# Kernel optimization log

Measured on AMD Instinct MI355X. Metric: run time of the kernel, lower is better.

Reference implementation:

```python
import jax, jax.numpy as jnp
import numpy as np

H, W, C, B = 16, 16, 2048, 32
HEADS = 4
D1, D2 = 256, 128


def _build_edges(h, w):
    """Lattice + mirror + disease-node + self-loop edges (PyG GATConv default adds self loops)."""
    idx = lambda i, j: i * w + j
    edges = []
    for i in range(h):
        for j in range(w):
            if i + 1 < h:
                edges += [(idx(i, j), idx(i + 1, j)), (idx(i + 1, j), idx(i, j))]
            if j + 1 < w:
                edges += [(idx(i, j), idx(i, j + 1)), (idx(i, j + 1), idx(i, j))]
            mj = w - j - 1
            if mj != j:
                edges.append((idx(i, j), idx(i, mj)))
    n = h * w
    for i in range(n):  # disease node (index n), bidirectional
        edges += [(i, n), (n, i)]
    for i in range(n + 1):  # self loops
        edges.append((i, i))
    e = np.asarray(edges, dtype=np.int32)
    return jnp.asarray(e[:, 0]), jnp.asarray(e[:, 1])


def setup_inputs() -> dict:
    key = jax.random.key(0)
    ks = jax.random.split(key, 16)
    s = 0.02
    src, dst = _build_edges(H, W)
    return {
        "fmap": jax.random.normal(ks[0], (B, C, H, W), jnp.float32),
        "W1": jax.random.normal(ks[1], (C, HEADS * D1), jnp.float32) * s,
        "a_src1": jax.random.normal(ks[2], (HEADS, D1), jnp.float32) * s,
        "a_dst1": jax.random.normal(ks[3], (HEADS, D1), jnp.float32) * s,
        "b1": jnp.zeros((D1,), jnp.float32),
        "W2": jax.random.normal(ks[4], (D1, HEADS * D2), jnp.float32) * s,
        "a_src2": jax.random.normal(ks[5], (HEADS, D2), jnp.float32) * s,
        "a_dst2": jax.random.normal(ks[6], (HEADS, D2), jnp.float32) * s,
        "b2": jnp.zeros((D2,), jnp.float32),
        "Wp": jax.random.normal(ks[7], (D2, 1), jnp.float32) * s,
        "bp": jnp.zeros((1,), jnp.float32),
        "Wc1": jax.random.normal(ks[8], (D2, 64), jnp.float32) * s,
        "bc1": jnp.zeros((64,), jnp.float32),
        "Wc2": jax.random.normal(ks[9], (64, 1), jnp.float32) * s,
        "bc2": jnp.zeros((1,), jnp.float32),
        "src": src,
        "dst": dst,
    }


def _gat_layer(x, src, dst, Wm, a_s, a_d, b, heads, out_dim):
    """PyG GATConv math: concat=False (mean over heads), leaky_relu slope 0.2."""
    N = x.shape[0]
    h = (x @ Wm).reshape(N, heads, out_dim)           # [N, H, D]
    es = jnp.sum(h * a_s, axis=-1)                    # [N, H]
    ed = jnp.sum(h * a_d, axis=-1)                    # [N, H]
    e = jax.nn.leaky_relu(es[src] + ed[dst], 0.2)     # [E, H]
    m = jax.ops.segment_max(e, dst, num_segments=N)   # softmax over incoming edges
    alpha = jnp.exp(e - m[dst])
    denom = jax.ops.segment_sum(alpha, dst, num_segments=N)
    alpha = alpha / (denom[dst] + 1e-16)
    agg = jax.ops.segment_sum(alpha[:, :, None] * h[src], dst, num_segments=N)
    return agg.mean(axis=1) + b                       # [N, D]


def reference(fmap, W1, a_src1, a_dst1, b1, W2, a_src2, a_dst2, b2,
              Wp, bp, Wc1, bc1, Wc2, bc2, src, dst):
    Bn, Cc, Hh, Ww = fmap.shape
    nodes = fmap.reshape(Bn, Cc, Hh * Ww).transpose(0, 2, 1)   # [B, HW, C]
    nodes = jnp.concatenate([nodes, jnp.zeros((Bn, 1, Cc), nodes.dtype)], axis=1)

    def per_graph(x):
        x = _gat_layer(x, src, dst, W1, a_src1, a_dst1, b1, HEADS, D1)
        x = _gat_layer(x, src, dst, W2, a_src2, a_dst2, b2, HEADS, D2)
        w = jax.nn.sigmoid(x @ Wp + bp)               # [N, 1] attention pool weights
        g = jnp.mean(x * w, axis=0)                   # global_mean_pool, single graph
        h1 = jax.nn.relu(g @ Wc1 + bc1)
        pred = jax.nn.sigmoid(h1 @ Wc2 + bc2)         # [1]
        return pred[0], w[:, 0]

    preds, atts = jax.vmap(per_graph)(nodes)          # [B], [B, N]
    return preds, atts
```

## Files before the change

### kernel.cpp

```cpp
#include <hip/hip_runtime.h>

typedef __bf16 bf16_t;
typedef __bf16 bf16x8 __attribute__((ext_vector_type(8)));
typedef float f32x4 __attribute__((ext_vector_type(4)));

#define MPAD  8320
#define NNODE 257
#define NB    32

__device__ __forceinline__ void gld_lds16(const bf16_t* g, bf16_t* l) {
    __builtin_amdgcn_global_load_lds(
        (const __attribute__((address_space(1))) void*)g,
        (__attribute__((address_space(3))) void*)l, 16, 0, 0);
}

__global__ __launch_bounds__(256) void setup_kernel(const float* __restrict__ W1, bf16_t* __restrict__ W1t,
                                                    const float* __restrict__ W2, bf16_t* __restrict__ W2t,
                                                    const float* __restrict__ fmap, bf16_t* __restrict__ X,
                                                    const int* __restrict__ dstv, int E,
                                                    int* __restrict__ indptr, int* __restrict__ eidx,
                                                    float* __restrict__ zbase, bf16_t* __restrict__ out1) {
    __shared__ float smem[64 * 65];
    int idx = blockIdx.x, t = threadIdx.x;
    if (idx < 2176) {
        const float* W; bf16_t* Wt; int K, N, kt, nt;
        if (idx < 2048) { W = W1; Wt = W1t; K = 2048; N = 1024; kt = idx >> 5; nt = idx & 31; }
        else { int l = idx - 2048; W = W2; Wt = W2t; K = 256; N = 512; kt = l >> 4; nt = l & 15; }
        int k0 = kt * 32, n0 = nt * 32;
        int tx = t & 31, ty = t >> 5;
#pragma unroll
        for (int i = 0; i < 4; i++)
            smem[(ty + i * 8) * 33 + tx] = W[(size_t)(k0 + ty + i * 8) * N + n0 + tx];
        __syncthreads();
#pragma unroll
        for (int i = 0; i < 4; i++)
            Wt[(size_t)(n0 + ty + i * 8) * K + k0 + tx] = (bf16_t)smem[tx * 33 + ty + i * 8];
    } else if (idx < 6272) {
        int local = idx - 2176;
        int ct = local & 31, rem = local >> 5;
        int nt = rem & 3, b = rem >> 2;
        int c0 = ct * 64, n0 = nt * 64;
        const float* f = fmap + (size_t)b * 2048 * 256;
        int ln = t & 63, lc = t >> 6;
#pragma unroll
        for (int i = 0; i < 16; i++) {
            int c = lc + i * 4;
            smem[c * 65 + ln] = f[(size_t)(c0 + c) * 256 + n0 + ln];
        }
        __syncthreads();
        int sn = t >> 3, sc = (t & 7) * 8;
#pragma unroll
        for (int half = 0; half < 2; half++) {
            int n = sn + half * 32;
            bf16_t tmp[8];
#pragma unroll
            for (int j = 0; j < 8; j++) tmp[j] = (bf16_t)smem[(sc + j) * 65 + n];
            *(bf16x8*)&X[(size_t)(b * 257 + n0 + n) * 2048 + c0 + sc] = *(bf16x8*)tmp;
        }
    } else if (idx < 6402) {
        int local = idx - 6272;
        uint4* p = (uint4*)zbase + (size_t)local * 256;
        p[t] = uint4{0, 0, 0, 0};
    } else if (idx < 6530) {
        int i = idx - 6402;
        int row = (i < 32) ? (i * 257 + 256) : (8224 + (i - 32));
        uint4* p = (uint4*)(X + (size_t)row * 2048);
        p[t] = uint4{0, 0, 0, 0};
    } else if (idx < 6542) {
        int local = idx - 6530;
        uint4* p = (uint4*)((char*)(out1 + (size_t)8224 * 256) + (size_t)local * 4096);
        p[t] = uint4{0, 0, 0, 0};
    } else {
        __shared__ int cnt[258];
        __shared__ int off[258];
        for (int i = t; i < 258; i += 256) cnt[i] = 0;
        __syncthreads();
        for (int e = t; e < E; e += 256) atomicAdd(&cnt[dstv[e] + 1], 1);
        __syncthreads();
        if (t == 0) {
            int s = 0;
            for (int i = 0; i < 258; i++) { s += cnt[i]; off[i] = s; }
        }
        __syncthreads();
        for (int i = t; i < 258; i += 256) indptr[i] = off[i];
        __syncthreads();
        for (int e = t; e < E; e += 256) {
            int p = atomicAdd(&off[dstv[e]], 1);
            eidx[p] = e;
        }
    }
}

__global__ __launch_bounds__(128, 2) void gemm_kernel(const bf16_t* __restrict__ A,
                                                      const bf16_t* __restrict__ Bt,
                                                      bf16_t* __restrict__ C,
                                                      const float* __restrict__ asrc,
                                                      const float* __restrict__ adst,
                                                      float* __restrict__ es,
                                                      float* __restrict__ ed,
                                                      int K, int N, int headD) {
    __shared__ __align__(16) bf16_t sm[3 * 8192];
    int row0 = blockIdx.y * 128, col0 = blockIdx.x * 128;
    int t = threadIdx.x;
    int wave = t >> 6, lane = t & 63;
    int srow = lane >> 2, scol = (lane & 3) * 8;
    const bf16_t* Abase = A + (size_t)row0 * K;
    const bf16_t* Bbase = Bt + (size_t)col0 * K;
    f32x4 acc[4][8] = {};
    int fr = lane & 15;
    int kq = (lane >> 4) * 8;
    int nk = K >> 5;
    auto issue = [&](int kt, int stage) {
        bf16_t* As = sm + stage * 8192;
        bf16_t* Bs = As + 4096;
        int k0 = kt << 5;
#pragma unroll
        for (int c = 0; c < 4; c++) {
            int chunk = wave * 4 + c;
            int row = chunk * 16 + srow;
            gld_lds16(Abase + (size_t)row * K + k0 + scol, &As[chunk * 512]);
            gld_lds16(Bbase + (size_t)row * K + k0 + scol, &Bs[chunk * 512]);
        }
    };
    issue(0, 0);
    if (nk > 1) issue(1, 1);
    for (int k = 0; k < nk; k++) {
        int cur = k % 3;
        if (k + 2 < nk) {
            issue(k + 2, (k + 2) % 3);
            asm volatile("s_waitcnt vmcnt(16)" ::: "memory");
        } else if (k + 1 < nk) {
            asm volatile("s_waitcnt vmcnt(8)" ::: "memory");
        } else {
            asm volatile("s_waitcnt vmcnt(0)" ::: "memory");
        }
        __builtin_amdgcn_s_barrier();
        const bf16_t* As = sm + cur * 8192;
        const bf16_t* Bs = As + 4096;
        bf16x8 af[4], bfv[8];
#pragma unroll
        for (int mr = 0; mr < 4; mr++)
            af[mr] = *(const bf16x8*)&As[(wave * 64 + mr * 16 + fr) * 32 + kq];
#pragma unroll
        for (int nc = 0; nc < 8; nc++)
            bfv[nc] = *(const bf16x8*)&Bs[(nc * 16 + fr) * 32 + kq];
#pragma unroll
        for (int mr = 0; mr < 4; mr++)
#pragma unroll
            for (int nc = 0; nc < 8; nc++)
                acc[mr][nc] = __builtin_amdgcn_mfma_f32_16x16x32_bf16(
                    af[mr], bfv[nc], acc[mr][nc], 0, 0, 0);
        asm volatile("s_waitcnt lgkmcnt(0)" ::: "memory");
        __builtin_amdgcn_s_barrier();
    }
#pragma unroll
    for (int mr = 0; mr < 4; mr++) {
        int crow = row0 + wave * 64 + mr * 16 + (lane >> 4) * 4;
#pragma unroll
        for (int nc = 0; nc < 8; nc++) {
            int ccol = col0 + nc * 16 + (lane & 15);
#pragma unroll
            for (int r = 0; r < 4; r++)
                C[(size_t)(crow + r) * N + ccol] = (bf16_t)acc[mr][nc][r];
        }
    }
    int h = col0 / headD;
    float as_v[8], ad_v[8];
#pragma unroll
    for (int nc = 0; nc < 8; nc++) {
        int ccol = col0 + nc * 16 + (lane & 15);
        as_v[nc] = asrc[ccol];
        ad_v[nc] = adst[ccol];
    }
#pragma unroll
    for (int mr = 0; mr < 4; mr++)
#pragma unroll
        for (int r = 0; r < 4; r++) {
            float ps = 0.f, pd = 0.f;
#pragma unroll
            for (int nc = 0; nc < 8; nc++) {
                float v = acc[mr][nc][r];
                ps += v * as_v[nc];
                pd += v * ad_v[nc];
            }
#pragma unroll
            for (int m = 1; m < 16; m <<= 1) {
                ps += __shfl_xor(ps, m);
                pd += __shfl_xor(pd, m);
            }
            if ((lane & 15) == 0) {
                int row = row0 + wave * 64 + mr * 16 + (lane >> 4) * 4 + r;
                atomicAdd(&es[row * 4 + h], ps);
                atomicAdd(&ed[row * 4 + h], pd);
            }
        }
}

template<int D>
__global__ __launch_bounds__(256) void attn_kernel(const bf16_t* __restrict__ Hb,
                                                   const float* __restrict__ es,
                                                   const float* __restrict__ ed,
                                                   const int* __restrict__ indptr,
                                                   const int* __restrict__ eidx,
                                                   const int* __restrict__ srcv,
                                                   const float* __restrict__ bias,
                                                   float* __restrict__ outf,
                                                   bf16_t* __restrict__ outb) {
    constexpr int VPL = D / 64;
    int d = blockIdx.x, b = blockIdx.y;
    int r = b * 257 + d;
    int t = threadIdx.x, wv = t >> 6, lane = t & 63;
    int e0 = indptr[d];
    int deg = indptr[d + 1] - e0;
    __shared__ float alpha[NNODE * 4];
    __shared__ int   ssh[NNODE];
    __shared__ float wred[4][8];
    __shared__ float mh4[4], rh4[4];
    __shared__ float osh[4][D];
    const float4 edv = *(const float4*)&ed[r * 4];
    float edh[4] = {edv.x, edv.y, edv.z, edv.w};
    float lmax[4] = {-1e30f, -1e30f, -1e30f, -1e30f};
    for (int i = t; i < deg; i += 256) {
        int s = srcv[eidx[e0 + i]];
        ssh[i] = s;
        float4 e4 = *(const float4*)&es[(b * 257 + s) * 4];
        float ev[4] = {e4.x, e4.y, e4.z, e4.w};
#pragma unroll
        for (int h = 0; h < 4; h++) {
            float v = ev[h] + edh[h];
            v = v > 0.f ? v : 0.2f * v;
            alpha[i * 4 + h] = v;
            lmax[h] = fmaxf(lmax[h], v);
        }
    }
#pragma unroll
    for (int h = 0; h < 4; h++) {
        float m = lmax[h];
#pragma unroll
        for (int o = 32; o > 0; o >>= 1) m = fmaxf(m, __shfl_down(m, o));
        if (lane == 0) wred[h][wv] = m;
    }
    __syncthreads();
    if (t < 4)
        mh4[t] = fmaxf(fmaxf(wred[t][0], wred[t][1]), fmaxf(wred[t][2], wred[t][3]));
    __syncthreads();
    float lsum[4] = {0.f, 0.f, 0.f, 0.f};
    for (int i = t; i < deg; i += 256) {
#pragma unroll
        for (int h = 0; h < 4; h++) {
            float a = __expf(alpha[i * 4 + h] - mh4[h]);
            alpha[i * 4 + h] = a;
            lsum[h] += a;
        }
    }
#pragma unroll
    for (int h = 0; h < 4; h++) {
        float s = lsum[h];
#pragma unroll
        for (int o = 32; o > 0; o >>= 1) s += __shfl_down(s, o);
        if (lane == 0) wred[h][wv] = s;
    }
    __syncthreads();
    if (t < 4)
        rh4[t] = 1.f / (wred[t][0] + wred[t][1] + wred[t][2] + wred[t][3] + 1e-16f);
    __syncthreads();
    float rh = rh4[wv];
    float acc[VPL] = {};
    const bf16_t* hb = Hb + (size_t)(b * 257) * 4 * D + wv * D + lane * VPL;
    for (int i = 0; i < deg; i++) {
        float a = alpha[i * 4 + wv] * rh;
        const bf16_t* hr = hb + (size_t)ssh[i] * 4 * D;
        bf16_t xv[VPL];
        __builtin_memcpy(xv, hr, VPL * 2);
#pragma unroll
        for (int v = 0; v < VPL; v++) acc[v] += a * (float)xv[v];
    }
#pragma unroll
    for (int v = 0; v < VPL; v++) osh[wv][lane * VPL + v] = acc[v];
    __syncthreads();
    if (t < D) {
        float o = (osh[0][t] + osh[1][t] + osh[2][t] + osh[3][t]) * 0.25f + bias[t];
        if (outb) outb[(size_t)r * D + t] = (bf16_t)o;
        else      outf[(size_t)r * D + t] = o;
    }
}

__global__ __launch_bounds__(256) void head_kernel(const float* __restrict__ out2,
                                                   const float* __restrict__ Wp,
                                                   const float* __restrict__ bp,
                                                   const float* __restrict__ Wc1,
                                                   const float* __restrict__ bc1,
                                                   const float* __restrict__ Wc2,
                                                   const float* __restrict__ bc2,
                                                   float* __restrict__ outp) {
    int b = blockIdx.x, t = threadIdx.x, wv = t >> 6, lane = t & 63;
    __shared__ float wsh[NNODE];
    __shared__ float gpart[2][128];
    __shared__ float gsh[128];
    __shared__ float h1[64];
    const float* X = out2 + (size_t)b * 257 * 128;
    float wp0 = Wp[lane], wp1 = Wp[64 + lane], bp0 = bp[0];
    for (int n = wv; n < 257; n += 4) {
        const float* xr = X + n * 128;
        float s = xr[lane] * wp0 + xr[64 + lane] * wp1;
#pragma unroll
        for (int o = 32; o > 0; o >>= 1) s += __shfl_down(s, o);
        if (lane == 0) {
            float wvv = 1.f / (1.f + __expf(-(s + bp0)));
            wsh[n] = wvv;
            outp[32 + b * 257 + n] = wvv;
        }
    }
    __syncthreads();
    {
        int dim = t & 127, half = t >> 7;
        float s = 0.f;
        for (int n = half; n < 257; n += 2) s += X[n * 128 + dim] * wsh[n];
        gpart[half][dim] = s;
    }
    __syncthreads();
    if (t < 128) gsh[t] = (gpart[0][t] + gpart[1][t]) * (1.f / 257.f);
    __syncthreads();
    if (t < 64) {
        float s = bc1[t];
        for (int k = 0; k < 128; k++) s += gsh[k] * Wc1[k * 64 + t];
        h1[t] = fmaxf(s, 0.f);
    }
    __syncthreads();
    if (t == 0) {
        float s = bc2[0];
        for (int j = 0; j < 64; j++) s += h1[j] * Wc2[j];
        outp[b] = 1.f / (1.f + expf(-s));
    }
}

extern "C" void kernel_launch(void* const* d_in, const int* in_sizes, int n_in,
                              void* d_out, int out_size, void* d_ws, size_t ws_size,
                              hipStream_t stream) {
    const float* fmap   = (const float*)d_in[0];
    const float* W1     = (const float*)d_in[1];
    const float* a_src1 = (const float*)d_in[2];
    const float* a_dst1 = (const float*)d_in[3];
    const float* b1     = (const float*)d_in[4];
    const float* W2     = (const float*)d_in[5];
    const float* a_src2 = (const float*)d_in[6];
    const float* a_dst2 = (const float*)d_in[7];
    const float* b2     = (const float*)d_in[8];
    const float* Wp     = (const float*)d_in[9];
    const float* bp     = (const float*)d_in[10];
    const float* Wc1    = (const float*)d_in[11];
    const float* bc1    = (const float*)d_in[12];
    const float* Wc2    = (const float*)d_in[13];
    const float* bc2    = (const float*)d_in[14];
    const int*   srcv   = (const int*)d_in[15];
    const int*   dstv   = (const int*)d_in[16];
    int E = in_sizes[15];
    float* outp = (float*)d_out;

    char* w = (char*)d_ws;
    size_t off = 0;
    auto alloc = [&](size_t bytes) -> void* {
        void* p = w + off;
        off += (bytes + 255) & ~(size_t)255;
        return p;
    };
    bf16_t* X    = (bf16_t*)alloc((size_t)MPAD * 2048 * sizeof(bf16_t));
    bf16_t* W1t  = (bf16_t*)alloc((size_t)1024 * 2048 * sizeof(bf16_t));
    bf16_t* W2t  = (bf16_t*)alloc((size_t)512 * 256 * sizeof(bf16_t));
    bf16_t* H1   = (bf16_t*)alloc((size_t)MPAD * 1024 * sizeof(bf16_t));
    bf16_t* out1 = (bf16_t*)alloc((size_t)MPAD * 256 * sizeof(bf16_t));
    bf16_t* H2   = (bf16_t*)alloc((size_t)MPAD * 512 * sizeof(bf16_t));
    float*  out2 = (float*)alloc((size_t)MPAD * 128 * sizeof(float));
    float*  es1  = (float*)alloc((size_t)MPAD * 4 * sizeof(float));
    float*  ed1  = (float*)alloc((size_t)MPAD * 4 * sizeof(float));
    float*  es2  = (float*)alloc((size_t)MPAD * 4 * sizeof(float));
    float*  ed2  = (float*)alloc((size_t)MPAD * 4 * sizeof(float));
    int*  indptr = (int*)alloc(258 * sizeof(int));
    int*  eidx   = (int*)alloc((size_t)E * sizeof(int));

    setup_kernel<<<6543, 256, 0, stream>>>(W1, W1t, W2, W2t, fmap, X, dstv, E,
                                           indptr, eidx, es1, out1);
    gemm_kernel<<<dim3(1024 / 128, MPAD / 128), 128, 0, stream>>>(
        X, W1t, H1, a_src1, a_dst1, es1, ed1, 2048, 1024, 256);
    attn_kernel<256><<<dim3(NNODE, NB), 256, 0, stream>>>(H1, es1, ed1, indptr, eidx,
                                                          srcv, b1, nullptr, out1);
    gemm_kernel<<<dim3(512 / 128, MPAD / 128), 128, 0, stream>>>(
        out1, W2t, H2, a_src2, a_dst2, es2, ed2, 256, 512, 128);
    attn_kernel<128><<<dim3(NNODE, NB), 256, 0, stream>>>(H2, es2, ed2, indptr, eidx,
                                                          srcv, b2, out2, nullptr);
    head_kernel<<<NB, 256, 0, stream>>>(out2, Wp, bp, Wc1, bc1, Wc2, bc2, outp);

    (void)n_in; (void)out_size; (void)ws_size;
}
```

Before: 355.0 us.

## Retile GEMM to 128x64 with 256 threads, XCD-aware block remap, unroll attention gather

The GEMM tile shrinks from 128x128 with 2 waves to 128x64 with 4 waves, each wave owning 32 rows. The grid becomes a 1D launch remapped so consecutive tiles land on the same XCD. Launch bounds allow 4 blocks per CU. This gives more blocks and more occupancy, at the cost of less reuse per tile and a smaller MFMA block per wave. The attention aggregation loop is unrolled by 4 to issue several row gathers at once, and the softmax normalisation is moved out of the loop to a single multiply at the end.

```diff
diff --git a/kernel.cpp b/kernel.cpp
--- a/kernel.cpp
+++ b/kernel.cpp
@@ -91,36 +91,45 @@
     }
 }
 
-__global__ __launch_bounds__(128, 2) void gemm_kernel(const bf16_t* __restrict__ A,
+__global__ __launch_bounds__(256, 4) void gemm_kernel(const bf16_t* __restrict__ A,
                                                       const bf16_t* __restrict__ Bt,
                                                       bf16_t* __restrict__ C,
                                                       const float* __restrict__ asrc,
                                                       const float* __restrict__ adst,
                                                       float* __restrict__ es,
                                                       float* __restrict__ ed,
-                                                      int K, int N, int headD) {
-    __shared__ __align__(16) bf16_t sm[3 * 8192];
-    int row0 = blockIdx.y * 128, col0 = blockIdx.x * 128;
+                                                      int K, int N, int headD,
+                                                      int tiles_per_xcd, int ncol_log2) {
+    __shared__ __align__(16) bf16_t sm[3 * 6144];
+    int linear = blockIdx.x;
+    int gt = (linear & 7) * tiles_per_xcd + (linear >> 3);
+    int row0 = (gt >> ncol_log2) * 128;
+    int col0 = (gt & ((1 << ncol_log2) - 1)) * 64;
     int t = threadIdx.x;
     int wave = t >> 6, lane = t & 63;
     int srow = lane >> 2, scol = (lane & 3) * 8;
     const bf16_t* Abase = A + (size_t)row0 * K;
     const bf16_t* Bbase = Bt + (size_t)col0 * K;
-    f32x4 acc[4][8] = {};
+    const bf16_t* gsrc[3];
+    int ldsoff[3];
+#pragma unroll
+    for (int j = 0; j < 3; j++) {
+        int c = wave * 3 + j;
+        bool isB = c >= 8;
+        int cr = isB ? c - 8 : c;
+        gsrc[j] = (isB ? Bbase : Abase) + (size_t)(cr * 16 + srow) * K + scol;
+        ldsoff[j] = (isB ? 4096 : 0) + cr * 512;
+    }
+    f32x4 acc[2][4] = {};
     int fr = lane & 15;
     int kq = (lane >> 4) * 8;
     int nk = K >> 5;
     auto issue = [&](int kt, int stage) {
-        bf16_t* As = sm + stage * 8192;
-        bf16_t* Bs = As + 4096;
+        bf16_t* base = sm + stage * 6144;
         int k0 = kt << 5;
 #pragma unroll
-        for (int c = 0; c < 4; c++) {
-            int chunk = wave * 4 + c;
-            int row = chunk * 16 + srow;
-            gld_lds16(Abase + (size_t)row * K + k0 + scol, &As[chunk * 512]);
-            gld_lds16(Bbase + (size_t)row * K + k0 + scol, &Bs[chunk * 512]);
-        }
+        for (int j = 0; j < 3; j++)
+            gld_lds16(gsrc[j] + k0, base + ldsoff[j]);
     };
     issue(0, 0);
     if (nk > 1) issue(1, 1);
@@ -128,36 +137,36 @@
         int cur = k % 3;
         if (k + 2 < nk) {
             issue(k + 2, (k + 2) % 3);
-            asm volatile("s_waitcnt vmcnt(16)" ::: "memory");
+            asm volatile("s_waitcnt vmcnt(6)" ::: "memory");
         } else if (k + 1 < nk) {
-            asm volatile("s_waitcnt vmcnt(8)" ::: "memory");
+            asm volatile("s_waitcnt vmcnt(3)" ::: "memory");
         } else {
             asm volatile("s_waitcnt vmcnt(0)" ::: "memory");
         }
         __builtin_amdgcn_s_barrier();
-        const bf16_t* As = sm + cur * 8192;
+        const bf16_t* As = sm + cur * 6144;
         const bf16_t* Bs = As + 4096;
-        bf16x8 af[4], bfv[8];
-#pragma unroll
-        for (int mr = 0; mr < 4; mr++)
-            af[mr] = *(const bf16x8*)&As[(wave * 64 + mr * 16 + fr) * 32 + kq];
-#pragma unroll
-        for (int nc = 0; nc < 8; nc++)
+        bf16x8 af[2], bfv[4];
+#pragma unroll
+        for (int mr = 0; mr < 2; mr++)
+            af[mr] = *(const bf16x8*)&As[(wave * 32 + mr * 16 + fr) * 32 + kq];
+#pragma unroll
+        for (int nc = 0; nc < 4; nc++)
             bfv[nc] = *(const bf16x8*)&Bs[(nc * 16 + fr) * 32 + kq];
 #pragma unroll
-        for (int mr = 0; mr < 4; mr++)
-#pragma unroll
-            for (int nc = 0; nc < 8; nc++)
+        for (int mr = 0; mr < 2; mr++)
+#pragma unroll
+            for (int nc = 0; nc < 4; nc++)
                 acc[mr][nc] = __builtin_amdgcn_mfma_f32_16x16x32_bf16(
                     af[mr], bfv[nc], acc[mr][nc], 0, 0, 0);
         asm volatile("s_waitcnt lgkmcnt(0)" ::: "memory");
         __builtin_amdgcn_s_barrier();
     }
 #pragma unroll
-    for (int mr = 0; mr < 4; mr++) {
-        int crow = row0 + wave * 64 + mr * 16 + (lane >> 4) * 4;
-#pragma unroll
-        for (int nc = 0; nc < 8; nc++) {
+    for (int mr = 0; mr < 2; mr++) {
+        int crow = row0 + wave * 32 + mr * 16 + (lane >> 4) * 4;
+#pragma unroll
+        for (int nc = 0; nc < 4; nc++) {
             int ccol = col0 + nc * 16 + (lane & 15);
 #pragma unroll
             for (int r = 0; r < 4; r++)
@@ -165,20 +174,20 @@
         }
     }
     int h = col0 / headD;
-    float as_v[8], ad_v[8];
-#pragma unroll
-    for (int nc = 0; nc < 8; nc++) {
+    float as_v[4], ad_v[4];
+#pragma unroll
+    for (int nc = 0; nc < 4; nc++) {
         int ccol = col0 + nc * 16 + (lane & 15);
         as_v[nc] = asrc[ccol];
         ad_v[nc] = adst[ccol];
     }
 #pragma unroll
-    for (int mr = 0; mr < 4; mr++)
+    for (int mr = 0; mr < 2; mr++)
 #pragma unroll
         for (int r = 0; r < 4; r++) {
             float ps = 0.f, pd = 0.f;
 #pragma unroll
-            for (int nc = 0; nc < 8; nc++) {
+            for (int nc = 0; nc < 4; nc++) {
                 float v = acc[mr][nc][r];
                 ps += v * as_v[nc];
                 pd += v * ad_v[nc];
@@ -189,7 +198,7 @@
                 pd += __shfl_xor(pd, m);
             }
             if ((lane & 15) == 0) {
-                int row = row0 + wave * 64 + mr * 16 + (lane >> 4) * 4 + r;
+                int row = row0 + wave * 32 + mr * 16 + (lane >> 4) * 4 + r;
                 atomicAdd(&es[row * 4 + h], ps);
                 atomicAdd(&ed[row * 4 + h], pd);
             }
@@ -264,19 +273,36 @@
     if (t < 4)
         rh4[t] = 1.f / (wred[t][0] + wred[t][1] + wred[t][2] + wred[t][3] + 1e-16f);
     __syncthreads();
-    float rh = rh4[wv];
     float acc[VPL] = {};
     const bf16_t* hb = Hb + (size_t)(b * 257) * 4 * D + wv * D + lane * VPL;
-    for (int i = 0; i < deg; i++) {
-        float a = alpha[i * 4 + wv] * rh;
+    int i = 0;
+    for (; i + 4 <= deg; i += 4) {
+        float av[4];
+        const bf16_t* p[4];
+#pragma unroll
+        for (int u = 0; u < 4; u++) {
+            av[u] = alpha[(i + u) * 4 + wv];
+            p[u] = hb + (size_t)ssh[i + u] * 4 * D;
+        }
+        bf16_t xv[4][VPL];
+#pragma unroll
+        for (int u = 0; u < 4; u++) __builtin_memcpy(xv[u], p[u], VPL * 2);
+#pragma unroll
+        for (int u = 0; u < 4; u++)
+#pragma unroll
+            for (int v = 0; v < VPL; v++) acc[v] += av[u] * (float)xv[u][v];
+    }
+    for (; i < deg; i++) {
+        float a = alpha[i * 4 + wv];
         const bf16_t* hr = hb + (size_t)ssh[i] * 4 * D;
         bf16_t xv[VPL];
         __builtin_memcpy(xv, hr, VPL * 2);
 #pragma unroll
         for (int v = 0; v < VPL; v++) acc[v] += a * (float)xv[v];
     }
-#pragma unroll
-    for (int v = 0; v < VPL; v++) osh[wv][lane * VPL + v] = acc[v];
+    float rh = rh4[wv];
+#pragma unroll
+    for (int v = 0; v < VPL; v++) osh[wv][lane * VPL + v] = acc[v] * rh;
     __syncthreads();
     if (t < D) {
         float o = (osh[0][t] + osh[1][t] + osh[2][t] + osh[3][t]) * 0.25f + bias[t];
@@ -380,12 +406,12 @@
 
     setup_kernel<<<6543, 256, 0, stream>>>(W1, W1t, W2, W2t, fmap, X, dstv, E,
                                            indptr, eidx, es1, out1);
-    gemm_kernel<<<dim3(1024 / 128, MPAD / 128), 128, 0, stream>>>(
-        X, W1t, H1, a_src1, a_dst1, es1, ed1, 2048, 1024, 256);
+    gemm_kernel<<<1040, 256, 0, stream>>>(
+        X, W1t, H1, a_src1, a_dst1, es1, ed1, 2048, 1024, 256, 130, 4);
     attn_kernel<256><<<dim3(NNODE, NB), 256, 0, stream>>>(H1, es1, ed1, indptr, eidx,
                                                           srcv, b1, nullptr, out1);
-    gemm_kernel<<<dim3(512 / 128, MPAD / 128), 128, 0, stream>>>(
-        out1, W2t, H2, a_src2, a_dst2, es2, ed2, 256, 512, 128);
+    gemm_kernel<<<520, 256, 0, stream>>>(
+        out1, W2t, H2, a_src2, a_dst2, es2, ed2, 256, 512, 128, 65, 3);
     attn_kernel<128><<<dim3(NNODE, NB), 256, 0, stream>>>(H2, es2, ed2, indptr, eidx,
                                                           srcv, b2, out2, nullptr);
     head_kernel<<<NB, 256, 0, stream>>>(out2, Wp, bp, Wc1, bc1, Wc2, bc2, outp);
```

New measurement: 385.6 us. +8.6%, slower.
